# Performance work log

Hardware: AMD Instinct MI355X
Metric: run time of the kernel (lower is better)

The kernel has to match this reference:

```python
import math
import jax, jax.numpy as jnp
import numpy as np

C = 8.0  # decay constant from __init__
_MIN_RAD, _MAX_RAD = 0.9, 0.999


def block_diag_linear(x, w):
    # x: (B,T,D), w: (H, bs, bs) with D = H*bs
    B, T, D = x.shape
    H, bs, _ = w.shape
    xh = x.reshape(B, T, H, bs)
    return jnp.einsum('bthd,hde->bthe', xh, w).reshape(B, T, D)


def linear_scan(a, b):
    # h_t = a_t * h_{t-1} + b_t, h_{-1}=0, via associative scan:
    # (a1,b1) o (a2,b2) = (a1*a2, a2*b1 + b2)
    def op(l, r):
        a1, b1 = l
        a2, b2 = r
        return (a1 * a2, a2 * b1 + b2)
    return jax.lax.associative_scan(op, (a, b), axis=1)[1]


def setup_inputs() -> dict:
    key = jax.random.key(0)
    k1, k2, k3, k4 = jax.random.split(key, 4)
    B, T, D, H = 4, 4096, 1024, 8
    bs = D // H
    x = jax.random.normal(k1, (B, T, D), dtype=jnp.float32)
    std = 1.0 / math.sqrt(bs)
    w_in = jax.random.normal(k2, (H, bs, bs), dtype=jnp.float32) * std
    w_a = jax.random.normal(k3, (H, bs, bs), dtype=jnp.float32) * std
    # a_param init: softplus^{-1} of uniform in [-log(max_rad)/c, -log(min_rad)/c]
    sp = jax.random.uniform(k4, (D,), dtype=jnp.float32,
                            minval=-math.log(_MAX_RAD) / C,
                            maxval=-math.log(_MIN_RAD) / C)
    a_param = jnp.log(jnp.exp(sp) - 1.0 + 1e-8)
    return {"x": x, "a_param": a_param, "w_in": w_in, "w_a": w_a}


def reference(x, a_param, w_in, w_a):
    # RG-LRU forward with h_prev = None
    gate_x = jax.nn.sigmoid(block_diag_linear(x, w_in))  # input gate i_t
    gate_a = jax.nn.sigmoid(block_diag_linear(x, w_a))   # recurrence gate r_t
    log_a = -C * jax.nn.softplus(a_param) * gate_a       # (B,T,D)
    a = jnp.exp(log_a)
    multiplier = jnp.sqrt(1.0 - jnp.exp(2.0 * log_a))    # sqrt(1 - a^2)
    b = multiplier * (gate_x * x)
    y = linear_scan(a, b)                                 # (B,T,D)
    h_last = y[:, -1, :]
    return y, h_last
```

## Files before the change

kernel.cpp:

```cpp
#include <hip/hip_runtime.h>

#define B_ 4
#define T_ 4096
#define D_ 1024
#define H_ 8
#define CL2_ 16
#define NC2_ (T_/CL2_)
#define M_ (B_*T_)

typedef unsigned short u16;
typedef unsigned int u32;
typedef __attribute__((ext_vector_type(8))) short s16x8;
typedef __attribute__((ext_vector_type(4))) float f32x4;

#define LOG2E 1.4426950408889634f

__device__ __forceinline__ float ex2(float x){
#if __has_builtin(__builtin_amdgcn_exp2f)
  return __builtin_amdgcn_exp2f(x);
#else
  return exp2f(x);
#endif
}
__device__ __forceinline__ float rcpf(float x){
#if __has_builtin(__builtin_amdgcn_rcpf)
  return __builtin_amdgcn_rcpf(x);
#else
  return __fdividef(1.0f, x);
#endif
}
__device__ __forceinline__ float bf2f(u16 u){
  union { u32 i; float f; } v; v.i = ((u32)u) << 16; return v.f;
}
__device__ __forceinline__ u16 f2bf(float f){
  union { float f; u32 i; } v; v.f = f;
  u32 i = v.i;
  return (u16)((i + 0x7FFFu + ((i >> 16) & 1u)) >> 16);
}
__device__ __forceinline__ float sigf(float z){
  return rcpf(1.0f + ex2(-LOG2E * z));
}

__global__ __launch_bounds__(256) void k0_transpose(const float* __restrict__ w_in,
                                                    const float* __restrict__ w_a,
                                                    u16* __restrict__ wt){
  __shared__ float ls[128][132];
  const int blk = blockIdx.x;
  const float* src = (blk < 8 ? w_in : w_a) + (size_t)(blk & 7) * 128 * 128;
  u16* dst = wt + (size_t)blk * 128 * 128;
  const int tid = threadIdx.x;
  const int r0 = tid >> 5;
  const int c0 = (tid & 31) * 4;
  #pragma unroll
  for (int it = 0; it < 16; ++it){
    int r = r0 + it * 8;
    *(float4*)(&ls[r][c0]) = *(const float4*)(src + r * 128 + c0);
  }
  __syncthreads();
  #pragma unroll
  for (int it = 0; it < 16; ++it){
    int e = r0 + it * 8;
    ushort4 u;
    u.x = f2bf(ls[c0 + 0][e]);
    u.y = f2bf(ls[c0 + 1][e]);
    u.z = f2bf(ls[c0 + 2][e]);
    u.w = f2bf(ls[c0 + 3][e]);
    *(ushort4*)(dst + e * 128 + c0) = u;
  }
}

__global__ __launch_bounds__(256, 3) void k1_gemm(const float* __restrict__ x,
                                                  const float* __restrict__ a_param,
                                                  const u16* __restrict__ wt,
                                                  u32* __restrict__ pack,
                                                  float* __restrict__ carA,
                                                  float* __restrict__ carY){
  __shared__ u16 Xs[128][132];
  __shared__ float aspS[64];

  const int blk = blockIdx.x;
  const int h = blk & 7;
  const int eh = (blk >> 3) & 1;
  const int mbase = (blk >> 4) * 128;
  const int tid = threadIdx.x;

  {
    const int r0 = tid >> 5;
    const int c0 = (tid & 31) * 4;
    const float* xb = x + (size_t)mbase * D_ + h * 128;
    #pragma unroll
    for (int it = 0; it < 16; ++it){
      int r = r0 + it * 8;
      float4 v = *(const float4*)(xb + r * D_ + c0);
      ushort4 u;
      u.x = (u16)(__float_as_uint(v.x) >> 16);
      u.y = (u16)(__float_as_uint(v.y) >> 16);
      u.z = (u16)(__float_as_uint(v.z) >> 16);
      u.w = (u16)(__float_as_uint(v.w) >> 16);
      *(ushort4*)(&Xs[r][c0]) = u;
    }
  }
  if (tid < 64){
    float ap = a_param[h * 128 + eh * 64 + tid];
    aspS[tid] = 8.0f * log1pf(__expf(ap));
  }
  __syncthreads();

  const int wv = tid >> 6, lane = tid & 63;
  const int q = lane >> 4, l = lane & 15;

  f32x4 accX[2][4], accA[2][4];
  #pragma unroll
  for (int mt = 0; mt < 2; ++mt)
    #pragma unroll
    for (int nt = 0; nt < 4; ++nt){ accX[mt][nt] = (f32x4)0.0f; accA[mt][nt] = (f32x4)0.0f; }

  const u16* wbase = wt + (h * 128 + eh * 64 + l) * 128;
  #pragma unroll
  for (int kb = 0; kb < 4; ++kb){
    const int ko = kb * 32 + q * 8;
    s16x8 a0 = *(const s16x8*)(&Xs[wv * 32 + l][ko]);
    s16x8 a1 = *(const s16x8*)(&Xs[wv * 32 + 16 + l][ko]);
    #pragma unroll
    for (int nt = 0; nt < 4; ++nt){
      s16x8 bi = *(const s16x8*)(wbase + nt * 16 * 128 + ko);
      s16x8 ba = *(const s16x8*)(wbase + nt * 16 * 128 + ko + 8 * 128 * 128);
      accX[0][nt] = __builtin_amdgcn_mfma_f32_16x16x32_bf16(a0, bi, accX[0][nt], 0, 0, 0);
      accX[1][nt] = __builtin_amdgcn_mfma_f32_16x16x32_bf16(a1, bi, accX[1][nt], 0, 0, 0);
      accA[0][nt] = __builtin_amdgcn_mfma_f32_16x16x32_bf16(a0, ba, accA[0][nt], 0, 0, 0);
      accA[1][nt] = __builtin_amdgcn_mfma_f32_16x16x32_bf16(a1, ba, accA[1][nt], 0, 0, 0);
    }
  }

  const int batch = mbase >> 12;
  const int cwb = ((mbase & (T_ - 1)) >> 4) + wv * 2;
  #pragma unroll
  for (int mt = 0; mt < 2; ++mt){
    const int R0 = wv * 32 + mt * 16;
    #pragma unroll
    for (int nt = 0; nt < 4; ++nt){
      const int el = nt * 16 + l;
      const int col = eh * 64 + el;
      const float asp = aspS[el];
      float av[4], bvv[4];
      #pragma unroll
      for (int r = 0; r < 4; ++r){
        const int row = R0 + q * 4 + r;
        float gx = sigf(accX[mt][nt][r]);
        float ga = sigf(accA[mt][nt][r]);
        float la = -asp * ga;
        float a  = ex2(LOG2E * la);
        float mult = sqrtf(fmaxf(1.0f - a * a, 0.0f));
        float xv = bf2f(Xs[row][col]);
        float bv = mult * gx * xv;
        av[r] = a; bvv[r] = bv;
        pack[(mbase + row) * D_ + h * 128 + col] =
            (u32)f2bf(la) | ((u32)f2bf(bv) << 16);
      }
      float A = av[0] * av[1] * av[2] * av[3];
      float Y = bvv[0];
      Y = fmaf(av[1], Y, bvv[1]);
      Y = fmaf(av[2], Y, bvv[2]);
      Y = fmaf(av[3], Y, bvv[3]);
      float Ap = __shfl_xor(A, 16, 64);
      float Yp = __shfl_xor(Y, 16, 64);
      Y = (lane & 16) ? fmaf(A, Yp, Y) : fmaf(Ap, Y, Yp);
      A *= Ap;
      Ap = __shfl_xor(A, 32, 64);
      Yp = __shfl_xor(Y, 32, 64);
      Y = (lane & 32) ? fmaf(A, Yp, Y) : fmaf(Ap, Y, Yp);
      A *= Ap;
      if ((lane & 48) == 0){
        int ci = (batch * NC2_ + cwb + mt) * D_ + h * 128 + eh * 64 + nt * 16 + l;
        carA[ci] = A;
        carY[ci] = Y;
      }
    }
  }
}

__global__ __launch_bounds__(256) void k3_scan_carries(const float* __restrict__ carA,
                                                       const float* __restrict__ carY,
                                                       float* __restrict__ hin,
                                                       float* __restrict__ hlast){
  const int g = blockIdx.x * 256 + threadIdx.x;
  const int batch = g >> 10, d = g & 1023;
  float hcur = 0.0f;
  #pragma unroll 16
  for (int c = 0; c < NC2_; ++c){
    int ci = (batch * NC2_ + c) * D_ + d;
    float A = carA[ci], Y = carY[ci];
    hin[ci] = hcur;
    hcur = fmaf(A, hcur, Y);
  }
  hlast[batch * D_ + d] = hcur;
}

__global__ __launch_bounds__(256) void k2b_scan(const u32* pack,
                                               const float* __restrict__ hin,
                                               float* y_out){
  const int cg = blockIdx.x;
  const int d0 = threadIdx.x * 4;
  const int base = cg * (CL2_ * D_) + d0;
  float4 yv = *(const float4*)(&hin[cg * D_ + d0]);
  #pragma unroll
  for (int t = 0; t < CL2_; ++t){
    int idx = base + t * D_;
    uint4 w = *(const uint4*)(&pack[idx]);
    float a0 = ex2(LOG2E * bf2f((u16)(w.x & 0xFFFFu)));
    float a1 = ex2(LOG2E * bf2f((u16)(w.y & 0xFFFFu)));
    float a2 = ex2(LOG2E * bf2f((u16)(w.z & 0xFFFFu)));
    float a3 = ex2(LOG2E * bf2f((u16)(w.w & 0xFFFFu)));
    yv.x = fmaf(a0, yv.x, bf2f((u16)(w.x >> 16)));
    yv.y = fmaf(a1, yv.y, bf2f((u16)(w.y >> 16)));
    yv.z = fmaf(a2, yv.z, bf2f((u16)(w.z >> 16)));
    yv.w = fmaf(a3, yv.w, bf2f((u16)(w.w >> 16)));
    *(float4*)(&y_out[idx]) = yv;
  }
}

extern "C" void kernel_launch(void* const* d_in, const int* in_sizes, int n_in,
                              void* d_out, int out_size, void* d_ws, size_t ws_size,
                              hipStream_t stream) {
  const float* x    = (const float*)d_in[0];
  const float* ap   = (const float*)d_in[1];
  const float* w_in = (const float*)d_in[2];
  const float* w_a  = (const float*)d_in[3];
  float* y = (float*)d_out;
  float* hlast = y + (size_t)B_ * T_ * D_;
  u32* pack = (u32*)d_out;

  char* ws = (char*)d_ws;
  u16*   wt   = (u16*)(ws);
  float* carA = (float*)(ws + 524288);
  float* carY = (float*)(ws + 524288 + 4194304);
  float* hin  = (float*)(ws + 524288 + 8388608);

  k0_transpose<<<16, 256, 0, stream>>>(w_in, w_a, wt);
  k1_gemm<<<(M_ / 128) * H_ * 2, 256, 0, stream>>>(x, ap, wt, pack, carA, carY);
  k3_scan_carries<<<16, 256, 0, stream>>>(carA, carY, hin, hlast);
  k2b_scan<<<B_ * NC2_, 256, 0, stream>>>(pack, hin, y);
}
```

Measured before the change: 196.4 us.

## Stage weights in LDS and feed MFMA A-operands directly from global x

```diff
diff --git a/kernel.cpp b/kernel.cpp
--- a/kernel.cpp
+++ b/kernel.cpp
@@ -39,6 +39,18 @@
 }
 __device__ __forceinline__ float sigf(float z){
   return rcpf(1.0f + ex2(-LOG2E * z));
+}
+__device__ __forceinline__ s16x8 cvt8(float4 a, float4 b){
+  s16x8 r;
+  r[0] = (short)(__float_as_uint(a.x) >> 16);
+  r[1] = (short)(__float_as_uint(a.y) >> 16);
+  r[2] = (short)(__float_as_uint(a.z) >> 16);
+  r[3] = (short)(__float_as_uint(a.w) >> 16);
+  r[4] = (short)(__float_as_uint(b.x) >> 16);
+  r[5] = (short)(__float_as_uint(b.y) >> 16);
+  r[6] = (short)(__float_as_uint(b.z) >> 16);
+  r[7] = (short)(__float_as_uint(b.w) >> 16);
+  return r;
 }
 
 __global__ __launch_bounds__(256) void k0_transpose(const float* __restrict__ w_in,
@@ -69,13 +81,13 @@
   }
 }
 
-__global__ __launch_bounds__(256, 3) void k1_gemm(const float* __restrict__ x,
+__global__ __launch_bounds__(256, 2) void k1_gemm(const float* __restrict__ x,
                                                   const float* __restrict__ a_param,
                                                   const u16* __restrict__ wt,
                                                   u32* __restrict__ pack,
                                                   float* __restrict__ carA,
                                                   float* __restrict__ carY){
-  __shared__ u16 Xs[128][132];
+  __shared__ u16 wtS[2][64][136];
   __shared__ float aspS[64];
 
   const int blk = blockIdx.x;
@@ -83,48 +95,62 @@
   const int eh = (blk >> 3) & 1;
   const int mbase = (blk >> 4) * 128;
   const int tid = threadIdx.x;
+  const int wv = tid >> 6, lane = tid & 63;
+  const int q = lane >> 4, l = lane & 15;
 
   {
-    const int r0 = tid >> 5;
-    const int c0 = (tid & 31) * 4;
-    const float* xb = x + (size_t)mbase * D_ + h * 128;
-    #pragma unroll
-    for (int it = 0; it < 16; ++it){
-      int r = r0 + it * 8;
-      float4 v = *(const float4*)(xb + r * D_ + c0);
-      ushort4 u;
-      u.x = (u16)(__float_as_uint(v.x) >> 16);
-      u.y = (u16)(__float_as_uint(v.y) >> 16);
-      u.z = (u16)(__float_as_uint(v.z) >> 16);
-      u.w = (u16)(__float_as_uint(v.w) >> 16);
-      *(ushort4*)(&Xs[r][c0]) = u;
-    }
-  }
+    uint4 wbuf[8];
+    #pragma unroll
+    for (int it = 0; it < 8; ++it){
+      int idx = tid + it * 256;
+      int row = idx >> 4;
+      int mat = row >> 6, e = row & 63;
+      int c8 = (idx & 15) * 8;
+      wbuf[it] = *(const uint4*)(wt + (size_t)mat * (8 * 128 * 128)
+                                  + (h * 128 + eh * 64 + e) * 128 + c8);
+    }
+    #pragma unroll
+    for (int it = 0; it < 8; ++it){
+      int idx = tid + it * 256;
+      int row = idx >> 4;
+      int c8 = (idx & 15) * 8;
+      *(uint4*)(&wtS[0][0][0] + row * 136 + c8) = wbuf[it];
+    }
+  }
+
+  const float* xr0 = x + (size_t)(mbase + wv * 32 + l) * D_ + h * 128;
+  const float* xr1 = xr0 + 16 * D_;
+  float4 A0[4][2], A1[4][2];
+  #pragma unroll
+  for (int kb = 0; kb < 4; ++kb){
+    int ko = kb * 32 + q * 8;
+    A0[kb][0] = *(const float4*)(xr0 + ko);
+    A0[kb][1] = *(const float4*)(xr0 + ko + 4);
+    A1[kb][0] = *(const float4*)(xr1 + ko);
+    A1[kb][1] = *(const float4*)(xr1 + ko + 4);
+  }
+
   if (tid < 64){
     float ap = a_param[h * 128 + eh * 64 + tid];
     aspS[tid] = 8.0f * log1pf(__expf(ap));
   }
   __syncthreads();
 
-  const int wv = tid >> 6, lane = tid & 63;
-  const int q = lane >> 4, l = lane & 15;
-
   f32x4 accX[2][4], accA[2][4];
   #pragma unroll
   for (int mt = 0; mt < 2; ++mt)
     #pragma unroll
     for (int nt = 0; nt < 4; ++nt){ accX[mt][nt] = (f32x4)0.0f; accA[mt][nt] = (f32x4)0.0f; }
 
-  const u16* wbase = wt + (h * 128 + eh * 64 + l) * 128;
   #pragma unroll
   for (int kb = 0; kb < 4; ++kb){
     const int ko = kb * 32 + q * 8;
-    s16x8 a0 = *(const s16x8*)(&Xs[wv * 32 + l][ko]);
-    s16x8 a1 = *(const s16x8*)(&Xs[wv * 32 + 16 + l][ko]);
+    s16x8 a0 = cvt8(A0[kb][0], A0[kb][1]);
+    s16x8 a1 = cvt8(A1[kb][0], A1[kb][1]);
     #pragma unroll
     for (int nt = 0; nt < 4; ++nt){
-      s16x8 bi = *(const s16x8*)(wbase + nt * 16 * 128 + ko);
-      s16x8 ba = *(const s16x8*)(wbase + nt * 16 * 128 + ko + 8 * 128 * 128);
+      s16x8 bi = *(const s16x8*)(&wtS[0][nt * 16 + l][ko]);
+      s16x8 ba = *(const s16x8*)(&wtS[1][nt * 16 + l][ko]);
       accX[0][nt] = __builtin_amdgcn_mfma_f32_16x16x32_bf16(a0, bi, accX[0][nt], 0, 0, 0);
       accX[1][nt] = __builtin_amdgcn_mfma_f32_16x16x32_bf16(a1, bi, accX[1][nt], 0, 0, 0);
       accA[0][nt] = __builtin_amdgcn_mfma_f32_16x16x32_bf16(a0, ba, accA[0][nt], 0, 0, 0);
@@ -151,7 +177,7 @@
         float la = -asp * ga;
         float a  = ex2(LOG2E * la);
         float mult = sqrtf(fmaxf(1.0f - a * a, 0.0f));
-        float xv = bf2f(Xs[row][col]);
+        float xv = x[(size_t)(mbase + row) * D_ + h * 128 + col];
         float bv = mult * gx * xv;
         av[r] = a; bvv[r] = bv;
         pack[(mbase + row) * D_ + h * 128 + col] =
```

New measurement: 185.6 us. -5.5%, faster.
